# Kernel tuning notes

Hardware: AMD Instinct MI355X
Metric: run time of the kernel (lower is better)

Reference implementation:

```python
import jax, jax.numpy as jnp
import numpy as np


def setup_inputs() -> dict:
    key = jax.random.key(0)
    k1, k2 = jax.random.split(key)
    x = jax.random.normal(k1, (16384, 1024), dtype=jnp.float32)
    # 10 butterfly stages, each with 512 independent 2x2 mixing matrices
    Ws = jax.random.normal(k2, (10, 512, 2, 2), dtype=jnp.float32)
    return {"x": x, "Ws": Ws}


def reference(x, Ws):
    """PairLinear_MixerBlock forward for input_dim == output_dim == 2^L.
    selector and reducer are Identity; only the butterfly mixing stages remain.
    """
    bs, dim = x.shape
    n_stages = Ws.shape[0]  # log2(dim)
    y = x
    for i in range(n_stages):
        stride = 2 ** i
        # y.view(-1, 2, 2**i).permute(0, 2, 1).contiguous().view(bs, -1)
        y = y.reshape(-1, 2, stride).transpose(0, 2, 1).reshape(bs, -1)
        # PairLinear: view(bs, -1, 2) then per-pair 2x2 matmul with Ws[i]
        y = jnp.einsum('bpk,pkj->bpj', y.reshape(bs, -1, 2), Ws[i]).reshape(bs, -1)
        # y.view(-1, 2**i, 2).permute(0, 2, 1).contiguous()
        y = y.reshape(-1, stride, 2).transpose(0, 2, 1).reshape(bs, dim)
    return y
```

## Files before the change

### kernel.cpp

```cpp
#include <hip/hip_runtime.h>

#define DIM 1024
#define ROWS_PER_TILE 16

typedef float  f32x4  __attribute__((ext_vector_type(4)));
typedef short  bf16x8 __attribute__((ext_vector_type(8)));
typedef unsigned int u32x2 __attribute__((ext_vector_type(2)));
typedef unsigned int u32x4 __attribute__((ext_vector_type(4)));

#define WF_BYTES (2 * 32 * 2 * 64 * 16)


__device__ __forceinline__ short f2bfs(float f) {
    union { __bf16 b; short s; } c; c.b = (__bf16)f; return c.s;
}
__device__ __forceinline__ unsigned f2bfbits(float f) {
    union { __bf16 b; unsigned short u; } c; c.b = (__bf16)f; return (unsigned)c.u;
}
__device__ __forceinline__ float bfbits2f(unsigned bits16shifted) {
    union { unsigned u; float f; } c; c.u = bits16shifted; return c.f;
}

__global__ __launch_bounds__(64) void compose_pack(const float* __restrict__ Ws,
                                                   short* __restrict__ wf) {
    __shared__ float M[32 * 32];
    const int b = blockIdx.x;
    const int tid = threadIdx.x;
    const bool isB = b >= 32;
    const int grp = isB ? b - 32 : b;

    for (int s = tid; s < 1024; s += 64) M[s] = ((s >> 5) == (s & 31)) ? 1.f : 0.f;
    __syncthreads();

    for (int il = 0; il < 5; ++il) {
        #pragma unroll
        for (int s = 0; s < 8; ++s) {
            int task = tid + s * 64;
            int pl = task >> 5;
            int r  = task & 31;
            int lo = ((pl >> il) << (il + 1)) | (pl & ((1 << il) - 1));
            int hi = lo + (1 << il);
            int wi = isB ? ((5 + il) * 512 + pl * 32 + grp)
                         : (il * 512 + grp * 16 + pl);
            const float* W = Ws + (size_t)wi * 4;
            float w00 = W[0], w01 = W[1], w10 = W[2], w11 = W[3];
            float u = M[r * 32 + lo], v = M[r * 32 + hi];
            M[r * 32 + lo] = u * w00 + v * w10;
            M[r * 32 + hi] = u * w01 + v * w11;
        }
        __syncthreads();
    }

    const int q = tid >> 4, lr = tid & 15;
    #pragma unroll
    for (int nh = 0; nh < 2; ++nh) {
        bf16x8 fr;
        #pragma unroll
        for (int e = 0; e < 8; ++e)
            fr[e] = f2bfs(M[(q * 8 + e) * 32 + nh * 16 + lr]);
        size_t idx = (size_t)(isB ? 4096 : 0) + ((size_t)grp * 2 + nh) * 64 + tid;
        ((bf16x8*)wf)[idx] = fr;
    }
}

__global__ __launch_bounds__(256) void bfly_mfma(
    const float* __restrict__ x,
    const short* __restrict__ wf1,
    const short* __restrict__ wf2,
    float* __restrict__ out)
{
    __shared__ char zt[32 * 1024];
    const int tid = threadIdx.x;
    const int w = tid >> 6;
    const int l = tid & 63;
    const int q = l >> 4, lr = l & 15;
    const int row0 = blockIdx.x * ROWS_PER_TILE;

    const f32x4 zacc = {0.f, 0.f, 0.f, 0.f};

    const float* xrow = x + (size_t)(row0 + lr) * DIM;
    #pragma unroll
    for (int gi = 0; gi < 8; ++gi) {
        const int g = w * 8 + gi;
        const f32x4* xp = (const f32x4*)(xrow + g * 32 + q * 8);
        f32x4 xa = __builtin_nontemporal_load(xp);
        f32x4 xb = __builtin_nontemporal_load(xp + 1);
        bf16x8 af;
        af[0] = f2bfs(xa[0]); af[1] = f2bfs(xa[1]);
        af[2] = f2bfs(xa[2]); af[3] = f2bfs(xa[3]);
        af[4] = f2bfs(xb[0]); af[5] = f2bfs(xb[1]);
        af[6] = f2bfs(xb[2]); af[7] = f2bfs(xb[3]);
        bf16x8 b0 = ((const bf16x8*)wf1)[(g * 2 + 0) * 64 + l];
        bf16x8 b1 = ((const bf16x8*)wf1)[(g * 2 + 1) * 64 + l];
        f32x4 c0 = __builtin_amdgcn_mfma_f32_16x16x32_bf16(af, b0, zacc, 0, 0, 0);
        f32x4 c1 = __builtin_amdgcn_mfma_f32_16x16x32_bf16(af, b1, zacc, 0, 0, 0);
        #pragma unroll
        for (int nh = 0; nh < 2; ++nh) {
            f32x4 cc = nh ? c1 : c0;
            int c = nh * 16 + lr;
            unsigned lo = f2bfbits(cc[0]) | (f2bfbits(cc[1]) << 16);
            unsigned hi = f2bfbits(cc[2]) | (f2bfbits(cc[3]) << 16);
            int byteoff = (c * 1024 + g * 32 + q * 8) ^ ((c & 15) << 3);
            u32x2 pk = {lo, hi};
            *(u32x2*)(zt + byteoff) = pk;
        }
    }
    __syncthreads();

    f32x4 o[2][8];
    #pragma unroll
    for (int hh = 0; hh < 8; ++hh) {
        const int h = w * 8 + hh;
        bf16x8 a2;
        #pragma unroll
        for (int e = 0; e < 8; ++e) {
            int byteoff = (h * 1024 + (q * 8 + e) * 32 + lr * 2) ^ ((h & 15) << 3);
            union { unsigned short u; short s; } cv;
            cv.u = *(const unsigned short*)(zt + byteoff);
            a2[e] = cv.s;
        }
        bf16x8 b0 = ((const bf16x8*)wf2)[(h * 2 + 0) * 64 + l];
        bf16x8 b1 = ((const bf16x8*)wf2)[(h * 2 + 1) * 64 + l];
        o[0][hh] = __builtin_amdgcn_mfma_f32_16x16x32_bf16(b0, a2, zacc, 0, 0, 0);
        o[1][hh] = __builtin_amdgcn_mfma_f32_16x16x32_bf16(b1, a2, zacc, 0, 0, 0);
    }
    __syncthreads();

    #pragma unroll
    for (int nh = 0; nh < 2; ++nh) {
        #pragma unroll
        for (int i = 0; i < 4; ++i) {
            unsigned p0 = f2bfbits(o[nh][0][i]) | (f2bfbits(o[nh][1][i]) << 16);
            unsigned p1 = f2bfbits(o[nh][2][i]) | (f2bfbits(o[nh][3][i]) << 16);
            unsigned p2 = f2bfbits(o[nh][4][i]) | (f2bfbits(o[nh][5][i]) << 16);
            unsigned p3 = f2bfbits(o[nh][6][i]) | (f2bfbits(o[nh][7][i]) << 16);
            int colb = (nh * 16 + q * 4 + i) * 32 + w * 8;
            int u = lr * 128 + (colb >> 3);
            u ^= (u >> 7) & 7;
            u32x4 pk = {p0, p1, p2, p3};
            *(u32x4*)(zt + u * 16) = pk;
        }
    }
    __syncthreads();

    const int trow = tid >> 4;
    const int tcb  = tid & 15;
    float* orow = out + (size_t)(row0 + trow) * DIM;
    #pragma unroll
    for (int j = 0; j < 8; ++j) {
        int ucol = j * 16 + tcb;
        int u = trow * 128 + ucol;
        u ^= (u >> 7) & 7;
        u32x4 pk = *(const u32x4*)(zt + u * 16);
        f32x4 v0, v1;
        v0[0] = bfbits2f(pk[0] << 16); v0[1] = bfbits2f(pk[0] & 0xffff0000u);
        v0[2] = bfbits2f(pk[1] << 16); v0[3] = bfbits2f(pk[1] & 0xffff0000u);
        v1[0] = bfbits2f(pk[2] << 16); v1[1] = bfbits2f(pk[2] & 0xffff0000u);
        v1[2] = bfbits2f(pk[3] << 16); v1[3] = bfbits2f(pk[3] & 0xffff0000u);
        float* dst = orow + ucol * 8;
        *(f32x4*)dst = v0;
        *((f32x4*)dst + 1) = v1;
    }
}

__global__ __launch_bounds__(256) void butterfly_fallback(
    const float* __restrict__ x, const float* __restrict__ Ws,
    float* __restrict__ out, int rows)
{
    const int lane = threadIdx.x & 63;
    const int wave = threadIdx.x >> 6;
    const int row0 = (blockIdx.x * 4 + wave) * 2;
    const float4* __restrict__ Wm = (const float4*)Ws;
    float d[2][16];
    #pragma unroll
    for (int r = 0; r < 2; ++r) {
        int row = row0 + r;
        if (row < rows) {
            const f32x4* src = (const f32x4*)(x + (size_t)row * DIM);
            #pragma unroll
            for (int qq = 0; qq < 4; ++qq) {
                f32x4 v = src[qq * 64 + lane];
                d[r][qq*4+0]=v[0]; d[r][qq*4+1]=v[1]; d[r][qq*4+2]=v[2]; d[r][qq*4+3]=v[3];
            }
        } else { for (int e = 0; e < 16; ++e) d[r][e] = 0.f; }
    }
    #pragma unroll
    for (int qq = 0; qq < 4; ++qq) {
        int base = qq*128 + lane*2;
        float4 m0 = Wm[base], m1 = Wm[base+1];
        #pragma unroll
        for (int r = 0; r < 2; ++r) {
            int e = qq*4; float u,v;
            u=d[r][e+0]; v=d[r][e+1]; d[r][e+0]=u*m0.x+v*m0.z; d[r][e+1]=u*m0.y+v*m0.w;
            u=d[r][e+2]; v=d[r][e+3]; d[r][e+2]=u*m1.x+v*m1.z; d[r][e+3]=u*m1.y+v*m1.w;
        }
    }
    #pragma unroll
    for (int qq = 0; qq < 4; ++qq) {
        int base = 512 + qq*128 + lane*2;
        float4 m0 = Wm[base], m1 = Wm[base+1];
        #pragma unroll
        for (int r = 0; r < 2; ++r) {
            int e = qq*4; float u,v;
            u=d[r][e+0]; v=d[r][e+2]; d[r][e+0]=u*m0.x+v*m0.z; d[r][e+2]=u*m0.y+v*m0.w;
            u=d[r][e+1]; v=d[r][e+3]; d[r][e+1]=u*m1.x+v*m1.z; d[r][e+3]=u*m1.y+v*m1.w;
        }
    }
    #pragma unroll
    for (int i = 2; i < 8; ++i) {
        const int m = 1 << (i - 2);
        #pragma unroll
        for (int qq = 0; qq < 4; ++qq) {
            const int a = (lane >> (i - 2)) & 1;
            int P0 = (((qq*64 + lane) >> (i-1)) << i) | ((lane & (m-1)) << 2);
            int base = i*512 + P0;
            float4 M0 = Wm[base+0], M1 = Wm[base+1], M2 = Wm[base+2], M3 = Wm[base+3];
            float wA0 = a ? M0.w : M0.x, wB0 = a ? M0.y : M0.z;
            float wA1 = a ? M1.w : M1.x, wB1 = a ? M1.y : M1.z;
            float wA2 = a ? M2.w : M2.x, wB2 = a ? M2.y : M2.z;
            float wA3 = a ? M3.w : M3.x, wB3 = a ? M3.y : M3.z;
            #pragma unroll
            for (int r = 0; r < 2; ++r) {
                int e = qq*4;
                float o0=__shfl_xor(d[r][e+0],m), o1=__shfl_xor(d[r][e+1],m);
                float o2=__shfl_xor(d[r][e+2],m), o3=__shfl_xor(d[r][e+3],m);
                d[r][e+0]=d[r][e+0]*wA0+o0*wB0; d[r][e+1]=d[r][e+1]*wA1+o1*wB1;
                d[r][e+2]=d[r][e+2]*wA2+o2*wB2; d[r][e+3]=d[r][e+3]*wA3+o3*wB3;
            }
        }
    }
    #pragma unroll
    for (int qp = 0; qp < 2; ++qp) {
        int base = 8*512 + qp*256 + lane*4;
        float4 M0 = Wm[base+0], M1 = Wm[base+1], M2 = Wm[base+2], M3 = Wm[base+3];
        #pragma unroll
        for (int r = 0; r < 2; ++r) {
            int eu=(2*qp)*4, ev=(2*qp+1)*4; float u,v;
            u=d[r][eu+0]; v=d[r][ev+0]; d[r][eu+0]=u*M0.x+v*M0.z; d[r][ev+0]=u*M0.y+v*M0.w;
            u=d[r][eu+1]; v=d[r][ev+1]; d[r][eu+1]=u*M1.x+v*M1.z; d[r][ev+1]=u*M1.y+v*M1.w;
            u=d[r][eu+2]; v=d[r][ev+2]; d[r][eu+2]=u*M2.x+v*M2.z; d[r][ev+2]=u*M2.y+v*M2.w;
            u=d[r][eu+3]; v=d[r][ev+3]; d[r][eu+3]=u*M3.x+v*M3.z; d[r][ev+3]=u*M3.y+v*M3.w;
        }
    }
    #pragma unroll
    for (int qp = 0; qp < 2; ++qp) {
        int base = 9*512 + qp*256 + lane*4;
        float4 M0 = Wm[base+0], M1 = Wm[base+1], M2 = Wm[base+2], M3 = Wm[base+3];
        #pragma unroll
        for (int r = 0; r < 2; ++r) {
            int eu=qp*4, ev=(qp+2)*4; float u,v;
            u=d[r][eu+0]; v=d[r][ev+0]; d[r][eu+0]=u*M0.x+v*M0.z; d[r][ev+0]=u*M0.y+v*M0.w;
            u=d[r][eu+1]; v=d[r][ev+1]; d[r][eu+1]=u*M1.x+v*M1.z; d[r][ev+1]=u*M1.y+v*M1.w;
            u=d[r][eu+2]; v=d[r][ev+2]; d[r][eu+2]=u*M2.x+v*M2.z; d[r][ev+2]=u*M2.y+v*M2.w;
            u=d[r][eu+3]; v=d[r][ev+3]; d[r][eu+3]=u*M3.x+v*M3.z; d[r][ev+3]=u*M3.y+v*M3.w;
        }
    }
    #pragma unroll
    for (int r = 0; r < 2; ++r) {
        int row = row0 + r;
        if (row < rows) {
            f32x4* dst = (f32x4*)(out + (size_t)row * DIM);
            #pragma unroll
            for (int qq = 0; qq < 4; ++qq) {
                f32x4 v = { d[r][qq*4+0], d[r][qq*4+1], d[r][qq*4+2], d[r][qq*4+3] };
                dst[qq * 64 + lane] = v;
            }
        }
    }
}

extern "C" void kernel_launch(void* const* d_in, const int* in_sizes, int n_in,
                              void* d_out, int out_size, void* d_ws, size_t ws_size,
                              hipStream_t stream) {
    const float* x  = (const float*)d_in[0];
    const float* Ws = (const float*)d_in[1];
    float* out = (float*)d_out;
    int rows = in_sizes[0] / DIM;

    if (ws_size >= (size_t)WF_BYTES && (rows % ROWS_PER_TILE) == 0) {
        short* wf1 = (short*)d_ws;
        short* wf2 = (short*)d_ws + 32768;
        compose_pack<<<64, 64, 0, stream>>>(Ws, (short*)d_ws);
        bfly_mfma<<<rows / ROWS_PER_TILE, 256, 0, stream>>>(x, wf1, wf2, out);
    } else {
        int grid = (rows + 7) / 8;
        butterfly_fallback<<<grid, 256, 0, stream>>>(x, Ws, out, rows);
    }
}
```

Before: 46.53 us.

## Restructure LDS layout for vectorized transposes and hoist global loads

All global loads of the input tile are issued up front into registers before any MFMA work. The first MFMA's operands are swapped so each lane's output fragments can be packed into full 16-byte vectors. This replaces the scattered 2-byte LDS reads in stage two with single 16-byte reads under a new XOR swizzle. The output staging layout is also re-swizzled so each wave writes a disjoint LDS region, which lets one __syncthreads be removed. The costs are higher register pressure from the 16 buffered input vectors and a write-back order that touches memory in smaller contiguous runs.

```diff
diff --git a/kernel.cpp b/kernel.cpp
--- a/kernel.cpp
+++ b/kernel.cpp
@@ -5,7 +5,6 @@
 
 typedef float  f32x4  __attribute__((ext_vector_type(4)));
 typedef short  bf16x8 __attribute__((ext_vector_type(8)));
-typedef unsigned int u32x2 __attribute__((ext_vector_type(2)));
 typedef unsigned int u32x4 __attribute__((ext_vector_type(4)));
 
 #define WF_BYTES (2 * 32 * 2 * 64 * 16)
@@ -79,12 +78,19 @@
     const f32x4 zacc = {0.f, 0.f, 0.f, 0.f};
 
     const float* xrow = x + (size_t)(row0 + lr) * DIM;
+    f32x4 xv[16];
+    #pragma unroll
+    for (int gi = 0; gi < 8; ++gi) {
+        const f32x4* xp = (const f32x4*)(xrow + (w * 8 + gi) * 32 + q * 8);
+        xv[2 * gi]     = __builtin_nontemporal_load(xp);
+        xv[2 * gi + 1] = __builtin_nontemporal_load(xp + 1);
+    }
+
+    bf16x8 zfr[2][4];
     #pragma unroll
     for (int gi = 0; gi < 8; ++gi) {
         const int g = w * 8 + gi;
-        const f32x4* xp = (const f32x4*)(xrow + g * 32 + q * 8);
-        f32x4 xa = __builtin_nontemporal_load(xp);
-        f32x4 xb = __builtin_nontemporal_load(xp + 1);
+        f32x4 xa = xv[2 * gi], xb = xv[2 * gi + 1];
         bf16x8 af;
         af[0] = f2bfs(xa[0]); af[1] = f2bfs(xa[1]);
         af[2] = f2bfs(xa[2]); af[3] = f2bfs(xa[3]);
@@ -92,17 +98,23 @@
         af[6] = f2bfs(xb[2]); af[7] = f2bfs(xb[3]);
         bf16x8 b0 = ((const bf16x8*)wf1)[(g * 2 + 0) * 64 + l];
         bf16x8 b1 = ((const bf16x8*)wf1)[(g * 2 + 1) * 64 + l];
-        f32x4 c0 = __builtin_amdgcn_mfma_f32_16x16x32_bf16(af, b0, zacc, 0, 0, 0);
-        f32x4 c1 = __builtin_amdgcn_mfma_f32_16x16x32_bf16(af, b1, zacc, 0, 0, 0);
-        #pragma unroll
-        for (int nh = 0; nh < 2; ++nh) {
-            f32x4 cc = nh ? c1 : c0;
-            int c = nh * 16 + lr;
-            unsigned lo = f2bfbits(cc[0]) | (f2bfbits(cc[1]) << 16);
-            unsigned hi = f2bfbits(cc[2]) | (f2bfbits(cc[3]) << 16);
-            int byteoff = (c * 1024 + g * 32 + q * 8) ^ ((c & 15) << 3);
-            u32x2 pk = {lo, hi};
-            *(u32x2*)(zt + byteoff) = pk;
+        f32x4 c0 = __builtin_amdgcn_mfma_f32_16x16x32_bf16(b0, af, zacc, 0, 0, 0);
+        f32x4 c1 = __builtin_amdgcn_mfma_f32_16x16x32_bf16(b1, af, zacc, 0, 0, 0);
+        #pragma unroll
+        for (int i = 0; i < 4; ++i) {
+            zfr[0][i][gi] = f2bfs(c0[i]);
+            zfr[1][i][gi] = f2bfs(c1[i]);
+        }
+    }
+
+    #pragma unroll
+    for (int nh = 0; nh < 2; ++nh) {
+        #pragma unroll
+        for (int i = 0; i < 4; ++i) {
+            int c = nh * 16 + q * 4 + i;
+            unsigned U = (unsigned)(c * 64 + lr * 4 + w);
+            U ^= (U >> 3) & 7;
+            *(bf16x8*)(zt + U * 16) = zfr[nh][i];
         }
     }
     __syncthreads();
@@ -111,20 +123,14 @@
     #pragma unroll
     for (int hh = 0; hh < 8; ++hh) {
         const int h = w * 8 + hh;
-        bf16x8 a2;
-        #pragma unroll
-        for (int e = 0; e < 8; ++e) {
-            int byteoff = (h * 1024 + (q * 8 + e) * 32 + lr * 2) ^ ((h & 15) << 3);
-            union { unsigned short u; short s; } cv;
-            cv.u = *(const unsigned short*)(zt + byteoff);
-            a2[e] = cv.s;
-        }
+        unsigned U = (unsigned)(h * 64 + lr * 4 + q);
+        U ^= (U >> 3) & 7;
+        bf16x8 a2 = *(const bf16x8*)(zt + U * 16);
         bf16x8 b0 = ((const bf16x8*)wf2)[(h * 2 + 0) * 64 + l];
         bf16x8 b1 = ((const bf16x8*)wf2)[(h * 2 + 1) * 64 + l];
         o[0][hh] = __builtin_amdgcn_mfma_f32_16x16x32_bf16(b0, a2, zacc, 0, 0, 0);
         o[1][hh] = __builtin_amdgcn_mfma_f32_16x16x32_bf16(b1, a2, zacc, 0, 0, 0);
     }
-    __syncthreads();
 
     #pragma unroll
     for (int nh = 0; nh < 2; ++nh) {
@@ -134,11 +140,12 @@
             unsigned p1 = f2bfbits(o[nh][2][i]) | (f2bfbits(o[nh][3][i]) << 16);
             unsigned p2 = f2bfbits(o[nh][4][i]) | (f2bfbits(o[nh][5][i]) << 16);
             unsigned p3 = f2bfbits(o[nh][6][i]) | (f2bfbits(o[nh][7][i]) << 16);
-            int colb = (nh * 16 + q * 4 + i) * 32 + w * 8;
-            int u = lr * 128 + (colb >> 3);
-            u ^= (u >> 7) & 7;
+            unsigned n = (unsigned)(nh * 16 + q * 4 + i);
+            unsigned U = (unsigned)(w * 512) + lr * 32 + n;
+            U ^= (U >> 5) & 7;
+            U ^= ((U >> 9) & 3) << 1;
             u32x4 pk = {p0, p1, p2, p3};
-            *(u32x4*)(zt + u * 16) = pk;
+            *(u32x4*)(zt + U * 16) = pk;
         }
     }
     __syncthreads();
@@ -147,17 +154,19 @@
     const int tcb  = tid & 15;
     float* orow = out + (size_t)(row0 + trow) * DIM;
     #pragma unroll
-    for (int j = 0; j < 8; ++j) {
-        int ucol = j * 16 + tcb;
-        int u = trow * 128 + ucol;
-        u ^= (u >> 7) & 7;
-        u32x4 pk = *(const u32x4*)(zt + u * 16);
+    for (int jp = 0; jp < 8; ++jp) {
+        int s = tcb >> 2, j = tcb & 3;
+        int n = jp * 4 + s;
+        unsigned U = (unsigned)(j * 512) + trow * 32 + n;
+        U ^= (U >> 5) & 7;
+        U ^= ((U >> 9) & 3) << 1;
+        u32x4 pk = *(const u32x4*)(zt + U * 16);
         f32x4 v0, v1;
         v0[0] = bfbits2f(pk[0] << 16); v0[1] = bfbits2f(pk[0] & 0xffff0000u);
         v0[2] = bfbits2f(pk[1] << 16); v0[3] = bfbits2f(pk[1] & 0xffff0000u);
         v1[0] = bfbits2f(pk[2] << 16); v1[1] = bfbits2f(pk[2] & 0xffff0000u);
         v1[2] = bfbits2f(pk[3] << 16); v1[3] = bfbits2f(pk[3] & 0xffff0000u);
-        float* dst = orow + ucol * 8;
+        float* dst = orow + n * 32 + j * 8;
         *(f32x4*)dst = v0;
         *((f32x4*)dst + 1) = v1;
     }
```

After: 50.49 us. 8.5% more time.
